# Kernel tuning notes

Measured on AMD Instinct MI355X. Metric: run time of the kernel, lower is better.

## Reference

```python
import jax, jax.numpy as jnp
import numpy as np

NUM_LAYERS = 16
IN_SIZE = 1024
OUT_SIZE = 1024
B, S = 64, 128

def setup_inputs() -> dict:
    key = jax.random.key(0)
    k1, k2, k3 = jax.random.split(key, 3)
    x = jax.random.normal(k1, (B, S, IN_SIZE), dtype=jnp.float32)
    layer_idx = jax.random.randint(k2, (S,), 0, NUM_LAYERS)
    weight = jax.random.normal(k3, (NUM_LAYERS, OUT_SIZE, IN_SIZE), dtype=jnp.float32)
    return {"x": x, "layer_idx": layer_idx, "weight": weight}

def reference(x, layer_idx, weight):
    # Branch: layer_idx is 1D with len == S (per-position weight selection).
    # Gather per-position weights [S, O, D] and do one batched contraction,
    # equivalent to the Python loop of per-step matmuls in the original.
    w = weight[layer_idx]                       # [S, O, D]
    out = jnp.einsum('bsd,sod->bso', x, w)      # [B, S, O]
    return out
```

## Files before the change

kernel.cpp:

```cpp
#include <hip/hip_runtime.h>
#include <hip/hip_bf16.h>

#define B_ 64
#define S_ 128
#define D_ 1024
#define O_ 1024
#define L_ 16

typedef __bf16 bf16x8 __attribute__((ext_vector_type(8)));
typedef float f32x4 __attribute__((ext_vector_type(4)));

#define WS_W     0ull
#define WS_X     33554432ull
#define WS_P     50331648ull
#define WS_PAIRS (WS_P + 16ull)
#define WS_NEED  (WS_PAIRS + 72ull * 16ull)

__device__ __forceinline__ unsigned f2bf2(float a, float b) {
    union { float f; unsigned u; } x{a}, y{b};
    unsigned lo = x.u + 0x7FFFu + ((x.u >> 16) & 1u);
    unsigned hi = y.u + 0x7FFFu + ((y.u >> 16) & 1u);
    return (lo >> 16) | (hi & 0xFFFF0000u);
}

__device__ __forceinline__ void gload16(const void* g, void* l) {
    __builtin_amdgcn_global_load_lds(
        (const __attribute__((address_space(1))) void*)g,
        (__attribute__((address_space(3))) void*)l, 16, 0, 0);
}

__global__ __launch_bounds__(256) void moshi_convert(
    const float* __restrict__ x, const float* __restrict__ w,
    const int* __restrict__ lidx, unsigned char* __restrict__ ws) {
    if (blockIdx.x == 0 && threadIdx.x < 16) {
        int t = threadIdx.x;
        int cnt[16];
        #pragma unroll 1
        for (int m = 0; m < 16; ++m) cnt[m] = 0;
        for (int s = 0; s < S_; ++s) ++cnt[lidx[s]];
        int off = 0;
        for (int m = 0; m < t; ++m) off += (cnt[m] + 1) >> 1;
        int4* pairs = (int4*)(ws + WS_PAIRS);
        int k = 0, prev = -1;
        for (int s = 0; s < S_; ++s) {
            if (lidx[s] == t) {
                if (k & 1) pairs[off + (k >> 1)] = make_int4(prev, s, t, 0);
                prev = s; ++k;
            }
        }
        if (k & 1) pairs[off + (k >> 1)] = make_int4(prev, prev, t, 0);
        if (t == 0) {
            int tot = 0;
            for (int m = 0; m < 16; ++m) tot += (cnt[m] + 1) >> 1;
            *(int*)(ws + WS_P) = tot;
        }
    }
    unsigned i0 = blockIdx.x * 512u + threadIdx.x;
    if (blockIdx.x < 8192) {
        const float4* src = reinterpret_cast<const float4*>(w);
        uint2* dst = reinterpret_cast<uint2*>(ws + WS_W);
        float4 v0 = src[i0];
        float4 v1 = src[i0 + 256];
        dst[i0]       = make_uint2(f2bf2(v0.x, v0.y), f2bf2(v0.z, v0.w));
        dst[i0 + 256] = make_uint2(f2bf2(v1.x, v1.y), f2bf2(v1.z, v1.w));
    } else {
        const float4* src = reinterpret_cast<const float4*>(x);
        uint2* dst = reinterpret_cast<uint2*>(ws + WS_X);
        unsigned j = i0 - 4194304u;
        float4 v0 = src[j];
        float4 v1 = src[j + 256];
        unsigned b0 = j >> 15, s0 = (j >> 8) & 127u, d40 = j & 255u;
        dst[(s0 * 64u + b0) * 256u + d40] =
            make_uint2(f2bf2(v0.x, v0.y), f2bf2(v0.z, v0.w));
        unsigned j1 = j + 256u;
        unsigned b1 = j1 >> 15, s1 = (j1 >> 8) & 127u, d41 = j1 & 255u;
        dst[(s1 * 64u + b1) * 256u + d41] =
            make_uint2(f2bf2(v1.x, v1.y), f2bf2(v1.z, v1.w));
    }
}

__global__ __launch_bounds__(512, 4) void moshi_gemm_n128(
    const unsigned char* __restrict__ ws, float* __restrict__ out) {
    __shared__ __align__(16) unsigned char lw[16384];
    __shared__ __align__(16) unsigned char lx[16384];

    const int bid = (blockIdx.x & 7) * 72 + (blockIdx.x >> 3);
    const int pi = bid >> 3;
    const int nt = bid & 7;
    const int np = *reinterpret_cast<const int*>(ws + WS_P);
    if (pi >= np) return;
    const int4 pr = *reinterpret_cast<const int4*>(ws + WS_PAIRS + 16ull * pi);
    const int s0 = pr.x, s1 = pr.y, l = pr.z;

    const int tid = threadIdx.x, lane = tid & 63, wid = tid >> 6;

    const int rowq = tid >> 3;
    const int c16  = (tid & 7) << 4;
    const int csw  = c16 ^ ((rowq & 7) << 4);
    const unsigned char* wsrc0 = ws + WS_W
        + ((size_t)(l * 1024 + nt * 128 + rowq) << 11) + csw;
    const unsigned char* wsrc1 = wsrc0 + ((size_t)64 << 11);
    const unsigned char* xsrc0 = ws + WS_X + ((size_t)(s0 * 64 + rowq) << 11) + csw;
    const unsigned char* xsrc1 = ws + WS_X + ((size_t)(s1 * 64 + rowq) << 11) + csw;

    const int wm = wid >> 2, wn = wid & 3;
    const int swz = (lane & 7) << 4;
    const int kb  = (lane >> 4) << 4;
    const int a_base = (wm * 64 + (lane & 15)) * 128 + kb;
    const int b_base = (wn * 32 + (lane & 15)) * 128 + kb;

    f32x4 acc[4][2];
    #pragma unroll
    for (int i = 0; i < 4; ++i)
        #pragma unroll
        for (int j = 0; j < 2; ++j) acc[i][j] = (f32x4)0.0f;

    #pragma unroll 1
    for (int kt = 0; kt < 16; ++kt) {
        __syncthreads();
        gload16(wsrc0 + kt * 128, lw + tid * 16);
        gload16(wsrc1 + kt * 128, lw + tid * 16 + 8192);
        gload16(xsrc0 + kt * 128, lx + tid * 16);
        gload16(xsrc1 + kt * 128, lx + tid * 16 + 8192);
        __syncthreads();
        #pragma unroll
        for (int kk = 0; kk < 2; ++kk) {
            bf16x8 af[4], bfr[2];
            #pragma unroll
            for (int mi = 0; mi < 4; ++mi)
                af[mi] = *reinterpret_cast<const bf16x8*>(
                    lx + (((a_base + kk * 64) ^ swz) + mi * 2048));
            #pragma unroll
            for (int ni = 0; ni < 2; ++ni)
                bfr[ni] = *reinterpret_cast<const bf16x8*>(
                    lw + (((b_base + kk * 64) ^ swz) + ni * 2048));
            #pragma unroll
            for (int mi = 0; mi < 4; ++mi)
                #pragma unroll
                for (int ni = 0; ni < 2; ++ni)
                    acc[mi][ni] = __builtin_amdgcn_mfma_f32_16x16x32_bf16(
                        af[mi], bfr[ni], acc[mi][ni], 0, 0, 0);
        }
    }

    const int s_sel = wm ? s1 : s0;
    const int col0 = nt * 128 + wn * 32 + (lane & 15);
    const int r0 = (lane >> 4) << 2;
    #pragma unroll
    for (int mi = 0; mi < 4; ++mi)
        #pragma unroll
        for (int ni = 0; ni < 2; ++ni)
            #pragma unroll
            for (int r = 0; r < 4; ++r) {
                int b = mi * 16 + r0 + r;
                out[((size_t)b * S_ + s_sel) * O_ + col0 + ni * 16] = acc[mi][ni][r];
            }
}

__global__ __launch_bounds__(256) void moshi_flin_fallback(
    const float* __restrict__ x, const int* __restrict__ lidx,
    const float* __restrict__ w, float* __restrict__ out) {
    __shared__ __align__(16) unsigned char lxs[64 * 128];
    __shared__ __align__(16) unsigned char lws[128 * 128];
    const int bid = blockIdx.x;
    const int s = bid >> 3, n0 = (bid & 7) << 7;
    const int tid = threadIdx.x, lane = tid & 63, wid = tid >> 6;
    const int idx = lidx[s];
    const float* wb = w + (size_t)idx * O_ * D_ + (size_t)n0 * D_;
    const float* xb = x + (size_t)s * D_;
    const int swz = (lane & 7) << 4;
    const int kb = (lane >> 4) << 4;
    const int a_base = (lane & 15) * 128 + kb;
    const int b_base = (wid * 32 + (lane & 15)) * 128 + kb;
    f32x4 acc[4][2];
    #pragma unroll
    for (int i = 0; i < 4; ++i)
        #pragma unroll
        for (int j = 0; j < 2; ++j) acc[i][j] = (f32x4)0.0f;
    for (int kt = 0; kt < D_; kt += 64) {
        __syncthreads();
        #pragma unroll
        for (int p = 0; p < 4; ++p) {
            int f = tid + p * 256, row = f >> 4, cc = (f & 15) << 2;
            const float4 v = *reinterpret_cast<const float4*>(
                xb + (size_t)row * (S_ * D_) + kt + cc);
            uint2 pk = { f2bf2(v.x, v.y), f2bf2(v.z, v.w) };
            *reinterpret_cast<uint2*>(&lxs[(row * 128 + cc * 2) ^ ((row & 7) << 4)]) = pk;
        }
        #pragma unroll
        for (int p = 0; p < 8; ++p) {
            int f = tid + p * 256, row = f >> 4, cc = (f & 15) << 2;
            const float4 v = *reinterpret_cast<const float4*>(
                wb + (size_t)row * D_ + kt + cc);
            uint2 pk = { f2bf2(v.x, v.y), f2bf2(v.z, v.w) };
            *reinterpret_cast<uint2*>(&lws[(row * 128 + cc * 2) ^ ((row & 7) << 4)]) = pk;
        }
        __syncthreads();
        #pragma unroll
        for (int kk = 0; kk < 2; ++kk) {
            bf16x8 af[4], bfr[2];
            #pragma unroll
            for (int mi = 0; mi < 4; ++mi)
                af[mi] = *reinterpret_cast<const bf16x8*>(
                    &lxs[(((a_base + kk * 64) ^ swz) + mi * 2048)]);
            #pragma unroll
            for (int ni = 0; ni < 2; ++ni)
                bfr[ni] = *reinterpret_cast<const bf16x8*>(
                    &lws[(((b_base + kk * 64) ^ swz) + ni * 2048)]);
            #pragma unroll
            for (int mi = 0; mi < 4; ++mi)
                #pragma unroll
                for (int ni = 0; ni < 2; ++ni)
                    acc[mi][ni] = __builtin_amdgcn_mfma_f32_16x16x32_bf16(
                        af[mi], bfr[ni], acc[mi][ni], 0, 0, 0);
        }
    }
    float* ob = out + (size_t)s * O_ + n0 + wid * 32 + (lane & 15);
    const int r0 = (lane >> 4) << 2;
    #pragma unroll
    for (int mi = 0; mi < 4; ++mi)
        #pragma unroll
        for (int ni = 0; ni < 2; ++ni)
            #pragma unroll
            for (int r = 0; r < 4; ++r) {
                int b = mi * 16 + r0 + r;
                ob[(size_t)b * (S_ * O_) + ni * 16] = acc[mi][ni][r];
            }
}

extern "C" void kernel_launch(void* const* d_in, const int* in_sizes, int n_in,
                              void* d_out, int out_size, void* d_ws, size_t ws_size,
                              hipStream_t stream) {
    const float* x  = (const float*)d_in[0];
    const int* lidx = (const int*)d_in[1];
    const float* w  = (const float*)d_in[2];
    float* out      = (float*)d_out;

    if (ws_size < WS_NEED) {
        moshi_flin_fallback<<<dim3(128 * 8), dim3(256), 0, stream>>>(x, lidx, w, out);
        return;
    }
    unsigned char* ws = (unsigned char*)d_ws;
    moshi_convert<<<dim3(12288), dim3(256), 0, stream>>>(x, w, lidx, ws);
    moshi_gemm_n128<<<dim3(72 * 8), dim3(512), 0, stream>>>(ws, out);
}
```

Baseline: 56.45 us.

## Double-buffer LDS tiles with direct global-to-LDS prefetch two stages ahead

Replaces the single-buffered GEMM main loop with a two-buffer LDS pipeline. Each iteration loads all fragments for the current tile into registers, then reissues async global loads for tile kt+2 into the freed buffer, and raises wave priority around the MFMA block. Explicit vmcnt/lgkmcnt waits and raw barriers take the place of two __syncthreads per iteration, so load latency can overlap compute. LDS per block doubles to 64KB, which may lower occupancy below the 4-block launch bound. Correctness depends on the vmcnt counts matching the four loads issued per stage.

Result: faster. 55.26 us (-2.1%).

```diff
diff --git a/kernel.cpp b/kernel.cpp
--- a/kernel.cpp
+++ b/kernel.cpp
@@ -79,10 +79,9 @@
     }
 }
 
-__global__ __launch_bounds__(512, 4) void moshi_gemm_n128(
+__global__ __launch_bounds__(512, 4) void moshi_gemm_db(
     const unsigned char* __restrict__ ws, float* __restrict__ out) {
-    __shared__ __align__(16) unsigned char lw[16384];
-    __shared__ __align__(16) unsigned char lx[16384];
+    __shared__ __align__(16) unsigned char buf[2][32768];
 
     const int bid = (blockIdx.x & 7) * 72 + (blockIdx.x >> 3);
     const int pi = bid >> 3;
@@ -106,7 +105,7 @@
     const int wm = wid >> 2, wn = wid & 3;
     const int swz = (lane & 7) << 4;
     const int kb  = (lane >> 4) << 4;
-    const int a_base = (wm * 64 + (lane & 15)) * 128 + kb;
+    const int a_base = 16384 + (wm * 64 + (lane & 15)) * 128 + kb;
     const int b_base = (wn * 32 + (lane & 15)) * 128 + kb;
 
     f32x4 acc[4][2];
@@ -115,32 +114,58 @@
         #pragma unroll
         for (int j = 0; j < 2; ++j) acc[i][j] = (f32x4)0.0f;
 
+    auto STAGE = [&](int kt, int b) {
+        gload16(wsrc0 + kt * 128, buf[b] + tid * 16);
+        gload16(wsrc1 + kt * 128, buf[b] + tid * 16 + 8192);
+        gload16(xsrc0 + kt * 128, buf[b] + 16384 + tid * 16);
+        gload16(xsrc1 + kt * 128, buf[b] + 16384 + tid * 16 + 8192);
+    };
+
+    STAGE(0, 0);
+    STAGE(1, 1);
+    asm volatile("s_waitcnt vmcnt(4)" ::: "memory");
+    __builtin_amdgcn_s_barrier();
+
+    int cur = 0;
     #pragma unroll 1
     for (int kt = 0; kt < 16; ++kt) {
-        __syncthreads();
-        gload16(wsrc0 + kt * 128, lw + tid * 16);
-        gload16(wsrc1 + kt * 128, lw + tid * 16 + 8192);
-        gload16(xsrc0 + kt * 128, lx + tid * 16);
-        gload16(xsrc1 + kt * 128, lx + tid * 16 + 8192);
-        __syncthreads();
+        const unsigned char* bc = buf[cur];
+
+        bf16x8 af[2][4], bfr[2][2];
         #pragma unroll
         for (int kk = 0; kk < 2; ++kk) {
-            bf16x8 af[4], bfr[2];
-            #pragma unroll
-            for (int mi = 0; mi < 4; ++mi)
-                af[mi] = *reinterpret_cast<const bf16x8*>(
-                    lx + (((a_base + kk * 64) ^ swz) + mi * 2048));
+            #pragma unroll
+            for (int mi = 0; mi < 4; ++mi)
+                af[kk][mi] = *reinterpret_cast<const bf16x8*>(
+                    bc + (((a_base + kk * 64) ^ swz) + mi * 2048));
             #pragma unroll
             for (int ni = 0; ni < 2; ++ni)
-                bfr[ni] = *reinterpret_cast<const bf16x8*>(
-                    lw + (((b_base + kk * 64) ^ swz) + ni * 2048));
+                bfr[kk][ni] = *reinterpret_cast<const bf16x8*>(
+                    bc + (((b_base + kk * 64) ^ swz) + ni * 2048));
+        }
+        asm volatile("s_waitcnt lgkmcnt(0)" ::: "memory");
+        __builtin_amdgcn_sched_barrier(0);
+        __builtin_amdgcn_s_barrier();
+
+        if (kt + 2 < 16) STAGE(kt + 2, cur);
+        __builtin_amdgcn_sched_barrier(0);
+
+        __builtin_amdgcn_s_setprio(1);
+        #pragma unroll
+        for (int kk = 0; kk < 2; ++kk)
             #pragma unroll
             for (int mi = 0; mi < 4; ++mi)
                 #pragma unroll
                 for (int ni = 0; ni < 2; ++ni)
                     acc[mi][ni] = __builtin_amdgcn_mfma_f32_16x16x32_bf16(
-                        af[mi], bfr[ni], acc[mi][ni], 0, 0, 0);
-        }
+                        af[kk][mi], bfr[kk][ni], acc[mi][ni], 0, 0, 0);
+        __builtin_amdgcn_s_setprio(0);
+
+        if (kt == 15) break;
+        if (kt + 2 < 16) asm volatile("s_waitcnt vmcnt(4)" ::: "memory");
+        else             asm volatile("s_waitcnt vmcnt(0)" ::: "memory");
+        __builtin_amdgcn_s_barrier();
+        cur ^= 1;
     }
 
     const int s_sel = wm ? s1 : s0;
@@ -242,5 +267,5 @@
     }
     unsigned char* ws = (unsigned char*)d_ws;
     moshi_convert<<<dim3(12288), dim3(256), 0, stream>>>(x, w, lidx, ws);
-    moshi_gemm_n128<<<dim3(72 * 8), dim3(512), 0, stream>>>(ws, out);
-}
+    moshi_gemm_db<<<dim3(72 * 8), dim3(512), 0, stream>>>(ws, out);
+}
```
